# Optimization experiments

Hardware: AMD Instinct MI355X
Metric: run time of the kernel (lower is better)

## Reference

```python
import jax
import jax.numpy as jnp
import numpy as np

B, S, D, H, HID, E, TOPK = 1, 2048, 1024, 16, 4096, 8, 2
HEAD_DIM = D // H


def _layer_norm(x, g, b, eps=1e-5):
    mu = jnp.mean(x, axis=-1, keepdims=True)
    var = jnp.var(x, axis=-1, keepdims=True)
    return (x - mu) * jax.lax.rsqrt(var + eps) * g + b


def setup_inputs() -> dict:
    key = jax.random.key(0)
    ks = jax.random.split(key, 12)
    s = 0.02
    return {
        "x": jax.random.normal(ks[0], (B, S, D), jnp.float32),
        "ln1_g": jnp.ones((D,), jnp.float32),
        "ln1_b": jnp.zeros((D,), jnp.float32),
        "wq": jax.random.normal(ks[1], (D, D), jnp.float32) * s,
        "wk": jax.random.normal(ks[2], (D, D), jnp.float32) * s,
        "wv": jax.random.normal(ks[3], (D, D), jnp.float32) * s,
        "wo": jax.random.normal(ks[4], (D, D), jnp.float32) * s,
        "ln2_g": jnp.ones((D,), jnp.float32),
        "ln2_b": jnp.zeros((D,), jnp.float32),
        "w_gate": jax.random.normal(ks[5], (D, E), jnp.float32) * s,
        "w_eg": jax.random.normal(ks[6], (E, D, HID), jnp.float32) * s,
        "w_eu": jax.random.normal(ks[7], (E, D, HID), jnp.float32) * s,
        "w_ed": jax.random.normal(ks[8], (E, HID, D), jnp.float32) * s,
    }


def _attention(h, wq, wk, wv, wo):
    b, s, d = h.shape
    q = (h @ wq).reshape(b, s, H, HEAD_DIM).transpose(0, 2, 1, 3)
    k = (h @ wk).reshape(b, s, H, HEAD_DIM).transpose(0, 2, 1, 3)
    v = (h @ wv).reshape(b, s, H, HEAD_DIM).transpose(0, 2, 1, 3)
    scores = jnp.einsum("bhqd,bhkd->bhqk", q, k) / jnp.sqrt(jnp.asarray(HEAD_DIM, h.dtype))
    causal = jnp.tril(jnp.ones((s, s), bool))  # [s,s]
    scores = jnp.where(causal, scores, jnp.asarray(-1e30, h.dtype))
    attn = jax.nn.softmax(scores, axis=-1)
    out = jnp.einsum("bhqk,bhkd->bhqd", attn, v).transpose(0, 2, 1, 3).reshape(b, s, d)
    return out @ wo


def _moe(h, w_gate, w_eg, w_eu, w_ed):
    b, s, d = h.shape
    flat = h.reshape(-1, d)  # [T,D]
    logits = flat @ w_gate  # [T,E]
    scores = jax.nn.sigmoid(logits)
    top_val, top_idx = jax.lax.top_k(scores, TOPK)
    top_val = top_val / (jnp.sum(top_val, axis=-1, keepdims=True) + 1e-9)
    # per-token per-expert combine weight (0 for unrouted experts)
    combine = jnp.sum(jax.nn.one_hot(top_idx, E, dtype=flat.dtype) * top_val[..., None], axis=1)  # [T,E]
    g = jax.nn.silu(jnp.einsum("td,edh->eth", flat, w_eg))
    u = jnp.einsum("td,edh->eth", flat, w_eu)
    eo = jnp.einsum("eth,ehd->etd", g * u, w_ed)  # [E,T,D]
    out = jnp.einsum("etd,te->td", eo, combine)
    return out.reshape(b, s, d)


def reference(x, ln1_g, ln1_b, wq, wk, wv, wo, ln2_g, ln2_b, w_gate, w_eg, w_eu, w_ed):
    x = x + _attention(_layer_norm(x, ln1_g, ln1_b), wq, wk, wv, wo)
    x = x + _moe(_layer_norm(x, ln2_g, ln2_b), w_gate, w_eg, w_eu, w_ed)
    return x
```

## Files before the change

kernel.cpp:

```cpp
#include <hip/hip_runtime.h>
#include <stdint.h>

#define DI __device__ __forceinline__

typedef short bf16x8_t __attribute__((ext_vector_type(8)));
typedef float f32x4_t __attribute__((ext_vector_type(4)));

DI unsigned short f2bf(float f) {
  union { float f; uint32_t u; } v; v.f = f;
  uint32_t u = v.u;
  u += 0x7fffu + ((u >> 16) & 1u);
  return (unsigned short)(u >> 16);
}

DI f32x4_t mfma16(bf16x8_t a, bf16x8_t b, f32x4_t c) {
  return __builtin_amdgcn_mfma_f32_16x16x32_bf16(a, b, c, 0, 0, 0);
}

DI void gload16(const void* g, void* l) {
  __builtin_amdgcn_global_load_lds(
      (const __attribute__((address_space(1))) uint32_t*)g,
      (__attribute__((address_space(3))) uint32_t*)l, 16, 0, 0);
}

__global__ __launch_bounds__(256) void transpose_cvt(const float* __restrict__ in,
                                                     unsigned short* __restrict__ out,
                                                     int R, int C) {
  __shared__ float tile[64][65];
  const int tid = threadIdx.x;
  const int tx = tid & 15, ty = tid >> 4;
  const size_t zoff = (size_t)blockIdx.z * R * C;
  const int r0 = blockIdx.y * 64, c0 = blockIdx.x * 64;
#pragma unroll
  for (int i = 0; i < 4; ++i) {
    const int r = ty + i * 16;
    const float4 v = *(const float4*)(in + zoff + (size_t)(r0 + r) * C + c0 + tx * 4);
    tile[r][tx * 4 + 0] = v.x; tile[r][tx * 4 + 1] = v.y;
    tile[r][tx * 4 + 2] = v.z; tile[r][tx * 4 + 3] = v.w;
  }
  __syncthreads();
#pragma unroll
  for (int i = 0; i < 4; ++i) {
    const int r = ty + i * 16;
    ushort4 o;
    o.x = f2bf(tile[tx * 4 + 0][r]); o.y = f2bf(tile[tx * 4 + 1][r]);
    o.z = f2bf(tile[tx * 4 + 2][r]); o.w = f2bf(tile[tx * 4 + 3][r]);
    *(ushort4*)(out + zoff + (size_t)(c0 + r) * R + r0 + tx * 4) = o;
  }
}

__global__ __launch_bounds__(256) void ln_kernel(const float* __restrict__ x, const float* __restrict__ g,
                                                 const float* __restrict__ b, unsigned short* __restrict__ out) {
  const int row = blockIdx.x, tid = threadIdx.x;
  const int wid = tid >> 6, lane = tid & 63;
  const float4 v = *(const float4*)(x + (size_t)row * 1024 + tid * 4);
  float s = v.x + v.y + v.z + v.w;
  float s2 = v.x * v.x + v.y * v.y + v.z * v.z + v.w * v.w;
#pragma unroll
  for (int o = 1; o < 64; o <<= 1) { s += __shfl_xor(s, o); s2 += __shfl_xor(s2, o); }
  __shared__ float red[8];
  if (lane == 0) { red[wid] = s; red[4 + wid] = s2; }
  __syncthreads();
  const float ts = red[0] + red[1] + red[2] + red[3];
  const float ts2 = red[4] + red[5] + red[6] + red[7];
  const float mu = ts * 0.0009765625f;
  const float var = ts2 * 0.0009765625f - mu * mu;
  const float rs = rsqrtf(var + 1e-5f);
  const float4 gg = *(const float4*)(g + tid * 4);
  const float4 bb = *(const float4*)(b + tid * 4);
  ushort4 o4;
  o4.x = f2bf((v.x - mu) * rs * gg.x + bb.x);
  o4.y = f2bf((v.y - mu) * rs * gg.y + bb.y);
  o4.z = f2bf((v.z - mu) * rs * gg.z + bb.z);
  o4.w = f2bf((v.w - mu) * rs * gg.w + bb.w);
  *(ushort4*)(out + (size_t)row * 1024 + tid * 4) = o4;
}

template<int BN>
DI void gemm_loop(const unsigned short* aR0, const unsigned short* aR1,
                  const unsigned short* bR0, const unsigned short* bR1,
                  const int K, unsigned short* lds, const int tid,
                  f32x4_t (&acc)[4][BN / 32]) {
  constexpr int NF = BN / 32;
  unsigned short* ldsA = lds;
  unsigned short* ldsB = lds + 4096;
  const int wid = tid >> 6, lane = tid & 63, ln = lane & 15, hi = lane >> 4;
  const int wr = wid >> 1, wc = wid & 1;
  char* dstA0 = (char*)ldsA + wid * 1024;
  char* dstA1 = (char*)ldsA + 4096 + wid * 1024;
  char* dstB0 = (char*)ldsB + wid * 1024;
  char* dstB1 = (char*)ldsB + 4096 + wid * 1024;
  for (int k0 = 0; k0 < K; k0 += 32) {
    gload16(aR0 + k0, dstA0);
    gload16(aR1 + k0, dstA1);
    gload16(bR0 + k0, dstB0);
    if constexpr (BN == 128) gload16(bR1 + k0, dstB1);
    __syncthreads();
    bf16x8_t af[4];
#pragma unroll
    for (int mf = 0; mf < 4; ++mf)
      af[mf] = *(const bf16x8_t*)&ldsA[(wr * 64 + mf * 16 + ln) * 32 + hi * 8];
#pragma unroll
    for (int nf = 0; nf < NF; ++nf) {
      bf16x8_t bfr = *(const bf16x8_t*)&ldsB[(wc * (BN / 2) + nf * 16 + ln) * 32 + hi * 8];
#pragma unroll
      for (int mf = 0; mf < 4; ++mf)
        acc[mf][nf] = mfma16(af[mf], bfr, acc[mf][nf]);
    }
    __syncthreads();
  }
}

__global__ __launch_bounds__(256) void qkv_kernel(const unsigned short* __restrict__ h1,
                                                  const unsigned short* __restrict__ wqT,
                                                  const unsigned short* __restrict__ wkT,
                                                  const unsigned short* __restrict__ wvT,
                                                  unsigned short* __restrict__ qb,
                                                  unsigned short* __restrict__ kbf,
                                                  unsigned short* __restrict__ vt) {
  __shared__ unsigned short lds[128 * 32 + 128 * 32];
  const int tid = threadIdx.x;
  const int z = blockIdx.z;
  const unsigned short* BT = (z == 0) ? wqT : (z == 1) ? wkT : wvT;
  const int m0 = blockIdx.y * 128, n0 = blockIdx.x * 128;
  f32x4_t acc[4][4] = {};
  const unsigned short* aR0 = h1 + (size_t)(m0 + (tid >> 2)) * 1024 + (tid & 3) * 8;
  const unsigned short* aR1 = aR0 + 64 * 1024;
  const unsigned short* bR0 = BT + (size_t)(n0 + (tid >> 2)) * 1024 + (tid & 3) * 8;
  const unsigned short* bR1 = bR0 + 64 * 1024;
  gemm_loop<128>(aR0, aR1, bR0, bR1, 1024, lds, tid, acc);
  const int lane = tid & 63, ln = lane & 15, hi = lane >> 4, wid = tid >> 6;
  const int wr = wid >> 1, wc = wid & 1;
  if (z < 2) {
    unsigned short* o = z ? kbf : qb;
#pragma unroll
    for (int mf = 0; mf < 4; ++mf)
#pragma unroll
      for (int nf = 0; nf < 4; ++nf)
#pragma unroll
        for (int r = 0; r < 4; ++r) {
          const int m = m0 + wr * 64 + mf * 16 + hi * 4 + r;
          const int n = n0 + wc * 64 + nf * 16 + ln;
          o[(size_t)m * 1024 + n] = f2bf(acc[mf][nf][r]);
        }
  } else {
#pragma unroll
    for (int mf = 0; mf < 4; ++mf)
#pragma unroll
      for (int nf = 0; nf < 4; ++nf) {
        const int n = n0 + wc * 64 + nf * 16 + ln;
        const int mb = m0 + wr * 64 + mf * 16 + hi * 4;
        ushort4 o;
        o.x = f2bf(acc[mf][nf][0]); o.y = f2bf(acc[mf][nf][1]);
        o.z = f2bf(acc[mf][nf][2]); o.w = f2bf(acc[mf][nf][3]);
        *(ushort4*)(vt + (size_t)n * 2048 + mb) = o;
      }
  }
}

__global__ __launch_bounds__(256) void wo_kernel(const unsigned short* __restrict__ ao,
                                                 const unsigned short* __restrict__ woT,
                                                 const float* __restrict__ x,
                                                 float* __restrict__ out) {
  __shared__ unsigned short lds[128 * 32 + 64 * 32];
  const int tid = threadIdx.x;
  const int m0 = blockIdx.y * 128, n0 = blockIdx.x * 64;
  f32x4_t acc[4][2] = {};
  const unsigned short* aR0 = ao + (size_t)(m0 + (tid >> 2)) * 1024 + (tid & 3) * 8;
  const unsigned short* aR1 = aR0 + 64 * 1024;
  const unsigned short* bR0 = woT + (size_t)(n0 + (tid >> 2)) * 1024 + (tid & 3) * 8;
  gemm_loop<64>(aR0, aR1, bR0, nullptr, 1024, lds, tid, acc);
  const int lane = tid & 63, ln = lane & 15, hi = lane >> 4, wid = tid >> 6;
  const int wr = wid >> 1, wc = wid & 1;
#pragma unroll
  for (int mf = 0; mf < 4; ++mf)
#pragma unroll
    for (int nf = 0; nf < 2; ++nf)
#pragma unroll
      for (int r = 0; r < 4; ++r) {
        const int m = m0 + wr * 64 + mf * 16 + hi * 4 + r;
        const int n = n0 + wc * 32 + nf * 16 + ln;
        out[(size_t)m * 1024 + n] = acc[mf][nf][r] + x[(size_t)m * 1024 + n];
      }
}

__global__ __launch_bounds__(256) void attn_kernel(const unsigned short* __restrict__ qb,
                                                   const unsigned short* __restrict__ kbuf,
                                                   const unsigned short* __restrict__ vt,
                                                   unsigned short* __restrict__ ao) {
  __shared__ unsigned short kTl[4096];
  __shared__ unsigned short vTl[4096];
  __shared__ unsigned short pl[4][1024];
  const int tid = threadIdx.x;
  const int wid = tid >> 6, lane = tid & 63;
  const int ln = lane & 15, hi = lane >> 4;
  const int h = blockIdx.y;
  const int q0 = blockIdx.x * 64;
  const int q0w = q0 + wid * 16;

  const unsigned short* qrow = qb + (size_t)(q0w + ln) * 1024 + h * 64 + hi * 8;
  const bf16x8_t aq0 = *(const bf16x8_t*)(qrow);
  const bf16x8_t aq1 = *(const bf16x8_t*)(qrow + 32);

  const int str_r = tid >> 3, str_c = tid & 7;
  const int swc = (str_c ^ (str_r & 7)) * 8;
  const unsigned short* ksrc0 = kbuf + (size_t)str_r * 1024 + h * 64 + swc;
  const unsigned short* ksrc1 = kbuf + (size_t)(str_r + 32) * 1024 + h * 64 + swc;
  const unsigned short* vsrc0 = vt + (size_t)(h * 64 + str_r) * 2048 + swc;
  const unsigned short* vsrc1 = vt + (size_t)(h * 64 + str_r + 32) * 2048 + swc;
  char* kd0 = (char*)kTl + wid * 1024;
  char* kd1 = (char*)kTl + 4096 + wid * 1024;
  char* vd0 = (char*)vTl + wid * 1024;
  char* vd1 = (char*)vTl + 4096 + wid * 1024;

  float m_r[4], l_r[4];
  f32x4_t o_acc[4] = {};
#pragma unroll
  for (int r = 0; r < 4; ++r) { m_r[r] = -1e30f; l_r[r] = 0.f; }

  const int nkv = blockIdx.x + 1;
  for (int it = 0; it < nkv; ++it) {
    const int kv0 = it * 64;
    gload16(ksrc0 + (size_t)kv0 * 1024, kd0);
    gload16(ksrc1 + (size_t)kv0 * 1024, kd1);
    gload16(vsrc0 + kv0, vd0);
    gload16(vsrc1 + kv0, vd1);
    __syncthreads();

    float sc[4][4];
#pragma unroll
    for (int cf = 0; cf < 4; ++cf) {
      const int row = cf * 16 + ln;
      const int swz = row & 7;
      const bf16x8_t b0 = *(const bf16x8_t*)((char*)kTl + row * 128 + ((hi ^ swz) * 16));
      const bf16x8_t b1 = *(const bf16x8_t*)((char*)kTl + row * 128 + (((4 + hi) ^ swz) * 16));
      f32x4_t zacc = {};
      zacc = mfma16(aq0, b0, zacc);
      zacc = mfma16(aq1, b1, zacc);
#pragma unroll
      for (int r = 0; r < 4; ++r) sc[cf][r] = zacc[r] * 0.125f;
    }
    if (kv0 + 63 > q0w) {
#pragma unroll
      for (int cf = 0; cf < 4; ++cf)
#pragma unroll
        for (int r = 0; r < 4; ++r) {
          const int qg = q0w + hi * 4 + r;
          const int kg = kv0 + cf * 16 + ln;
          if (kg > qg) sc[cf][r] = -1e30f;
        }
    }
#pragma unroll
    for (int r = 0; r < 4; ++r) {
      float tm = fmaxf(fmaxf(sc[0][r], sc[1][r]), fmaxf(sc[2][r], sc[3][r]));
      tm = fmaxf(tm, __shfl_xor(tm, 1));
      tm = fmaxf(tm, __shfl_xor(tm, 2));
      tm = fmaxf(tm, __shfl_xor(tm, 4));
      tm = fmaxf(tm, __shfl_xor(tm, 8));
      const float mn = fmaxf(m_r[r], tm);
      const float alpha = __expf(m_r[r] - mn);
      float rsum = 0.f;
#pragma unroll
      for (int cf = 0; cf < 4; ++cf) {
        const float p = __expf(sc[cf][r] - mn);
        sc[cf][r] = p; rsum += p;
      }
      rsum += __shfl_xor(rsum, 1); rsum += __shfl_xor(rsum, 2);
      rsum += __shfl_xor(rsum, 4); rsum += __shfl_xor(rsum, 8);
      l_r[r] = l_r[r] * alpha + rsum;
      m_r[r] = mn;
#pragma unroll
      for (int df = 0; df < 4; ++df) o_acc[df][r] *= alpha;
    }
    unsigned short* pw = &pl[wid][0];
#pragma unroll
    for (int cf = 0; cf < 4; ++cf)
#pragma unroll
      for (int r = 0; r < 4; ++r) {
        const int qq = hi * 4 + r;
        const int kv = cf * 16 + ln;
        const int bo = (qq * 128 + kv * 2) ^ ((qq & 7) << 4);
        *(unsigned short*)((char*)pw + bo) = f2bf(sc[cf][r]);
      }
    __syncthreads();
    const bf16x8_t pa0 = *(const bf16x8_t*)((char*)pw + ((ln * 128 + hi * 16) ^ ((ln & 7) << 4)));
    const bf16x8_t pa1 = *(const bf16x8_t*)((char*)pw + ((ln * 128 + 64 + hi * 16) ^ ((ln & 7) << 4)));
#pragma unroll
    for (int df = 0; df < 4; ++df) {
      const int d = df * 16 + ln;
      const int swz = d & 7;
      const bf16x8_t bv0 = *(const bf16x8_t*)((char*)vTl + d * 128 + ((hi ^ swz) * 16));
      const bf16x8_t bv1 = *(const bf16x8_t*)((char*)vTl + d * 128 + (((4 + hi) ^ swz) * 16));
      o_acc[df] = mfma16(pa0, bv0, o_acc[df]);
      o_acc[df] = mfma16(pa1, bv1, o_acc[df]);
    }
    __syncthreads();
  }
#pragma unroll
  for (int df = 0; df < 4; ++df) {
    const int n = h * 64 + df * 16 + ln;
#pragma unroll
    for (int r = 0; r < 4; ++r) {
      const int m = q0w + hi * 4 + r;
      ao[(size_t)m * 1024 + n] = f2bf(o_acc[df][r] / l_r[r]);
    }
  }
}

__global__ __launch_bounds__(256) void gate_kernel(const float* __restrict__ x2, const float* __restrict__ g,
                                                   const float* __restrict__ b, const float* __restrict__ wg,
                                                   int2* __restrict__ te, float2* __restrict__ tw,
                                                   int* __restrict__ cnt) {
  const int tid = threadIdx.x, wid = tid >> 6, lane = tid & 63;
  const int t = blockIdx.x * 4 + wid;
  const float* row = x2 + (size_t)t * 1024;
  float vv[16];
#pragma unroll
  for (int i = 0; i < 4; ++i) *(float4*)&vv[i * 4] = *(const float4*)(row + lane * 16 + i * 4);
  float s = 0.f, s2 = 0.f;
#pragma unroll
  for (int j = 0; j < 16; ++j) { s += vv[j]; s2 += vv[j] * vv[j]; }
#pragma unroll
  for (int o = 1; o < 64; o <<= 1) { s += __shfl_xor(s, o); s2 += __shfl_xor(s2, o); }
  const float mu = s * 0.0009765625f;
  const float var = s2 * 0.0009765625f - mu * mu;
  const float rs = rsqrtf(var + 1e-5f);
  float acc[8] = {0.f, 0.f, 0.f, 0.f, 0.f, 0.f, 0.f, 0.f};
#pragma unroll
  for (int j = 0; j < 16; ++j) {
    const int d = lane * 16 + j;
    const float xv = (vv[j] - mu) * rs * g[d] + b[d];
    const float4 w0 = *(const float4*)(wg + d * 8);
    const float4 w1 = *(const float4*)(wg + d * 8 + 4);
    acc[0] += xv * w0.x; acc[1] += xv * w0.y; acc[2] += xv * w0.z; acc[3] += xv * w0.w;
    acc[4] += xv * w1.x; acc[5] += xv * w1.y; acc[6] += xv * w1.z; acc[7] += xv * w1.w;
  }
#pragma unroll
  for (int o = 1; o < 64; o <<= 1) {
#pragma unroll
    for (int e = 0; e < 8; ++e) acc[e] += __shfl_xor(acc[e], o);
  }
  if (lane == 0) {
    float sg[8];
#pragma unroll
    for (int e = 0; e < 8; ++e) sg[e] = 1.f / (1.f + __expf(-acc[e]));
    int e0 = 0;
#pragma unroll
    for (int e = 1; e < 8; ++e) if (sg[e] > sg[e0]) e0 = e;
    int e1 = (e0 == 0) ? 1 : 0;
#pragma unroll
    for (int e = 0; e < 8; ++e) if (e != e0 && sg[e] > sg[e1]) e1 = e;
    const float v0 = sg[e0], v1 = sg[e1];
    const float inv = 1.f / (v0 + v1 + 1e-9f);
    te[t] = make_int2(e0, e1);
    tw[t] = make_float2(v0 * inv, v1 * inv);
    atomicAdd(&cnt[e0], 1);
    atomicAdd(&cnt[e1], 1);
  }
}

__global__ void zero_counters(int* p) { if (threadIdx.x < 8) p[threadIdx.x] = 0; }

__global__ void g2_kernel(const int* __restrict__ cnt, int* __restrict__ slot_off,
                          int* __restrict__ tile_expert, int* __restrict__ tile_rowbase,
                          int* __restrict__ cursor, int* __restrict__ assign_token,
                          float* __restrict__ assign_w) {
  const int tid = threadIdx.x;
  for (int i = tid; i < 5120; i += 64) { assign_token[i] = -1; assign_w[i] = 0.f; }
  if (tid == 0) {
    int base = 0, tiles = 0;
    for (int e = 0; e < 8; ++e) {
      const int c = cnt[e];
      slot_off[e] = base;
      cursor[e] = 0;
      const int nt = (c + 127) >> 7;
      for (int i = 0; i < nt; ++i) {
        tile_expert[tiles] = e;
        tile_rowbase[tiles] = base + i * 128;
        ++tiles;
      }
      base += nt * 128;
    }
    for (; tiles < 40; ++tiles) tile_expert[tiles] = -1;
  }
}

__global__ __launch_bounds__(256) void g3_kernel(const int2* __restrict__ te, const float2* __restrict__ tw,
                                                 const int* __restrict__ slot_off, int* __restrict__ cursor,
                                                 int* __restrict__ assign_token, float* __restrict__ assign_w) {
  const int t = blockIdx.x * 256 + threadIdx.x;
  const int2 e = te[t];
  const float2 w = tw[t];
  const int s0 = slot_off[e.x] + atomicAdd(&cursor[e.x], 1);
  assign_token[s0] = t; assign_w[s0] = w.x;
  const int s1 = slot_off[e.y] + atomicAdd(&cursor[e.y], 1);
  assign_token[s1] = t; assign_w[s1] = w.y;
}

__global__ __launch_bounds__(256) void upgate_kernel(const unsigned short* __restrict__ h2,
                                                     const float* __restrict__ w_eg, const float* __restrict__ w_eu,
                                                     const int* __restrict__ tile_expert,
                                                     const int* __restrict__ tile_rowbase,
                                                     const int* __restrict__ assign_token,
                                                     unsigned short* __restrict__ act) {
  const int by = blockIdx.y;
  const int e = tile_expert[by];
  if (e < 0) return;
  const int n0 = blockIdx.x * 64;
  const int rowbase = tile_rowbase[by];
  const int tid = threadIdx.x;
  __shared__ unsigned short lds[128 * 32 + 2 * 64 * 32];
  unsigned short* ldsA = lds;
  unsigned short* ldsB = lds + 4096;
  const int wid = tid >> 6, lane = tid & 63, ln = lane & 15, hi = lane >> 4;
  const int wr = wid >> 1, wc = wid & 1;
  const int r0s = rowbase + (tid >> 2);
  int t0 = assign_token[r0s];       t0 = t0 < 0 ? 0 : t0;
  int t1 = assign_token[r0s + 64];  t1 = t1 < 0 ? 0 : t1;
  const unsigned short* aR0 = h2 + (size_t)t0 * 1024 + (tid & 3) * 8;
  const unsigned short* aR1 = h2 + (size_t)t1 * 1024 + (tid & 3) * 8;
  char* dstA0 = (char*)ldsA + wid * 1024;
  char* dstA1 = (char*)ldsA + 4096 + wid * 1024;
  const int mat = tid >> 7;
  const int blk = tid & 127;
  const int kb = (blk >> 4) * 4;
  const int nb = (blk & 15) * 4;
  const float* bsrc = (mat ? w_eu : w_eg) + (size_t)e * 1024 * 4096 + (size_t)kb * 4096 + n0 + nb;
  unsigned short* bdst[4];
#pragma unroll
  for (int i = 0; i < 4; ++i) {
    const int n = nb + i;
    int bo = mat * 4096 + n * 64 + kb * 2;
    bo ^= ((n >> 2) & 3) << 4;
    bdst[i] = (unsigned short*)((char*)ldsB + bo);
  }
  f32x4_t accg[4][2] = {};
  f32x4_t accu[4][2] = {};
  for (int k0 = 0; k0 < 1024; k0 += 32) {
    gload16(aR0 + k0, dstA0);
    gload16(aR1 + k0, dstA1);
    const float* bs = bsrc + (size_t)k0 * 4096;
    const float4 q0 = *(const float4*)(bs);
    const float4 q1 = *(const float4*)(bs + 4096);
    const float4 q2 = *(const float4*)(bs + 8192);
    const float4 q3 = *(const float4*)(bs + 12288);
    ushort4 w0, w1, w2, w3;
    w0.x = f2bf(q0.x); w0.y = f2bf(q1.x); w0.z = f2bf(q2.x); w0.w = f2bf(q3.x);
    w1.x = f2bf(q0.y); w1.y = f2bf(q1.y); w1.z = f2bf(q2.y); w1.w = f2bf(q3.y);
    w2.x = f2bf(q0.z); w2.y = f2bf(q1.z); w2.z = f2bf(q2.z); w2.w = f2bf(q3.z);
    w3.x = f2bf(q0.w); w3.y = f2bf(q1.w); w3.z = f2bf(q2.w); w3.w = f2bf(q3.w);
    *(ushort4*)bdst[0] = w0; *(ushort4*)bdst[1] = w1;
    *(ushort4*)bdst[2] = w2; *(ushort4*)bdst[3] = w3;
    __syncthreads();
    bf16x8_t af[4];
#pragma unroll
    for (int mf = 0; mf < 4; ++mf)
      af[mf] = *(const bf16x8_t*)&ldsA[(wr * 64 + mf * 16 + ln) * 32 + hi * 8];
#pragma unroll
    for (int nf = 0; nf < 2; ++nf) {
      const int nrow = wc * 32 + nf * 16 + ln;
      int bo = nrow * 64 + hi * 16;
      bo ^= ((nrow >> 2) & 3) << 4;
      const bf16x8_t bg = *(const bf16x8_t*)((char*)ldsB + bo);
      const bf16x8_t bu = *(const bf16x8_t*)((char*)ldsB + 4096 + bo);
#pragma unroll
      for (int mf = 0; mf < 4; ++mf) {
        accg[mf][nf] = mfma16(af[mf], bg, accg[mf][nf]);
        accu[mf][nf] = mfma16(af[mf], bu, accu[mf][nf]);
      }
    }
    __syncthreads();
  }
#pragma unroll
  for (int mf = 0; mf < 4; ++mf)
#pragma unroll
    for (int nf = 0; nf < 2; ++nf)
#pragma unroll
      for (int r = 0; r < 4; ++r) {
        const int m = wr * 64 + mf * 16 + hi * 4 + r;
        const int n = n0 + wc * 32 + nf * 16 + ln;
        const float gv = accg[mf][nf][r], uv = accu[mf][nf][r];
        const float val = gv / (1.f + __expf(-gv)) * uv;
        act[(size_t)(rowbase + m) * 4096 + n] = f2bf(val);
      }
}

__global__ __launch_bounds__(256) void down_kernel(const unsigned short* __restrict__ act,
                                                   const float* __restrict__ w_ed,
                                                   const int* __restrict__ tile_expert,
                                                   const int* __restrict__ tile_rowbase,
                                                   const int* __restrict__ assign_token,
                                                   const float* __restrict__ assign_w,
                                                   float* __restrict__ out) {
  const int by = blockIdx.y;
  const int e = tile_expert[by];
  if (e < 0) return;
  const int n0 = blockIdx.x * 64;
  const int rowbase = tile_rowbase[by];
  const int tid = threadIdx.x;
  __shared__ unsigned short lds[128 * 32 + 64 * 32];
  unsigned short* ldsA = lds;
  unsigned short* ldsB = lds + 4096;
  const int wid = tid >> 6, lane = tid & 63, ln = lane & 15, hi = lane >> 4;
  const int wr = wid >> 1, wc = wid & 1;
  const unsigned short* aR0 = act + (size_t)(rowbase + (tid >> 2)) * 4096 + (tid & 3) * 8;
  const unsigned short* aR1 = aR0 + (size_t)64 * 4096;
  char* dstA0 = (char*)ldsA + wid * 1024;
  char* dstA1 = (char*)ldsA + 4096 + wid * 1024;
  const int blk = tid & 127;
  const int kb = (blk >> 4) * 4;
  const int nb = (blk & 15) * 4;
  const float* bsrc = w_ed + (size_t)e * 4096 * 1024 + (size_t)kb * 1024 + n0 + nb;
  unsigned short* bdst[4];
#pragma unroll
  for (int i = 0; i < 4; ++i) {
    const int n = nb + i;
    int bo = n * 64 + kb * 2;
    bo ^= ((n >> 2) & 3) << 4;
    bdst[i] = (unsigned short*)((char*)ldsB + bo);
  }
  f32x4_t acc[4][2] = {};
  for (int k0 = 0; k0 < 4096; k0 += 32) {
    gload16(aR0 + k0, dstA0);
    gload16(aR1 + k0, dstA1);
    if (tid < 128) {
      const float* bs = bsrc + (size_t)k0 * 1024;
      const float4 q0 = *(const float4*)(bs);
      const float4 q1 = *(const float4*)(bs + 1024);
      const float4 q2 = *(const float4*)(bs + 2048);
      const float4 q3 = *(const float4*)(bs + 3072);
      ushort4 w0, w1, w2, w3;
      w0.x = f2bf(q0.x); w0.y = f2bf(q1.x); w0.z = f2bf(q2.x); w0.w = f2bf(q3.x);
      w1.x = f2bf(q0.y); w1.y = f2bf(q1.y); w1.z = f2bf(q2.y); w1.w = f2bf(q3.y);
      w2.x = f2bf(q0.z); w2.y = f2bf(q1.z); w2.z = f2bf(q2.z); w2.w = f2bf(q3.z);
      w3.x = f2bf(q0.w); w3.y = f2bf(q1.w); w3.z = f2bf(q2.w); w3.w = f2bf(q3.w);
      *(ushort4*)bdst[0] = w0; *(ushort4*)bdst[1] = w1;
      *(ushort4*)bdst[2] = w2; *(ushort4*)bdst[3] = w3;
    }
    __syncthreads();
    bf16x8_t af[4];
#pragma unroll
    for (int mf = 0; mf < 4; ++mf)
      af[mf] = *(const bf16x8_t*)&ldsA[(wr * 64 + mf * 16 + ln) * 32 + hi * 8];
#pragma unroll
    for (int nf = 0; nf < 2; ++nf) {
      const int nrow = wc * 32 + nf * 16 + ln;
      int bo = nrow * 64 + hi * 16;
      bo ^= ((nrow >> 2) & 3) << 4;
      const bf16x8_t bb = *(const bf16x8_t*)((char*)ldsB + bo);
#pragma unroll
      for (int mf = 0; mf < 4; ++mf)
        acc[mf][nf] = mfma16(af[mf], bb, acc[mf][nf]);
    }
    __syncthreads();
  }
#pragma unroll
  for (int mf = 0; mf < 4; ++mf)
#pragma unroll
    for (int r = 0; r < 4; ++r) {
      const int m = wr * 64 + mf * 16 + hi * 4 + r;
      const int slot = rowbase + m;
      const int tk = assign_token[slot];
      if (tk >= 0) {
        const float w = assign_w[slot];
#pragma unroll
        for (int nf = 0; nf < 2; ++nf) {
          const int n = n0 + wc * 32 + nf * 16 + ln;
          atomicAdd(out + (size_t)tk * 1024 + n, acc[mf][nf][r] * w);
        }
      }
    }
}

extern "C" void kernel_launch(void* const* d_in, const int* in_sizes, int n_in,
                              void* d_out, int out_size, void* d_ws, size_t ws_size,
                              hipStream_t stream) {
  (void)in_sizes; (void)n_in; (void)out_size;
  const float* x    = (const float*)d_in[0];
  const float* ln1g = (const float*)d_in[1];
  const float* ln1b = (const float*)d_in[2];
  const float* wq   = (const float*)d_in[3];
  const float* wk   = (const float*)d_in[4];
  const float* wv   = (const float*)d_in[5];
  const float* wo   = (const float*)d_in[6];
  const float* ln2g = (const float*)d_in[7];
  const float* ln2b = (const float*)d_in[8];
  const float* wg   = (const float*)d_in[9];
  const float* weg  = (const float*)d_in[10];
  const float* weu  = (const float*)d_in[11];
  const float* wed  = (const float*)d_in[12];
  float* out = (float*)d_out;
  char* ws = (char*)d_ws;

  const size_t MB = (size_t)1 << 20;
  if (ws_size < 74 * MB) return;
  unsigned short* wqT = (unsigned short*)(ws + 0 * MB);
  unsigned short* wkT = (unsigned short*)(ws + 2 * MB);
  unsigned short* wvT = (unsigned short*)(ws + 4 * MB);
  unsigned short* woT = (unsigned short*)(ws + 6 * MB);
  unsigned short* h1  = (unsigned short*)(ws + 8 * MB);
  unsigned short* qb  = (unsigned short*)(ws + 12 * MB);
  unsigned short* kbf = (unsigned short*)(ws + 16 * MB);
  unsigned short* vt  = (unsigned short*)(ws + 20 * MB);
  unsigned short* ao  = (unsigned short*)(ws + 24 * MB);
  unsigned short* h2  = (unsigned short*)(ws + 28 * MB);
  unsigned short* act = (unsigned short*)(ws + 32 * MB);
  int2*   te = (int2*)(ws + 72 * MB);
  float2* tw = (float2*)(ws + 72 * MB + 16384);
  int*  meta = (int*)(ws + 72 * MB + 32768);
  int* cnt = meta;
  int* cursor = meta + 8;
  int* slot_off = meta + 16;
  int* tile_expert = meta + 24;
  int* tile_rowbase = meta + 64;
  int*   assign_token = (int*)(ws + 72 * MB + 36864);
  float* assign_w     = (float*)(ws + 72 * MB + 36864 + 20480);

  zero_counters<<<1, 64, 0, stream>>>(cnt);
  transpose_cvt<<<dim3(16, 16, 1), 256, 0, stream>>>(wq, wqT, 1024, 1024);
  transpose_cvt<<<dim3(16, 16, 1), 256, 0, stream>>>(wk, wkT, 1024, 1024);
  transpose_cvt<<<dim3(16, 16, 1), 256, 0, stream>>>(wv, wvT, 1024, 1024);
  transpose_cvt<<<dim3(16, 16, 1), 256, 0, stream>>>(wo, woT, 1024, 1024);
  ln_kernel<<<2048, 256, 0, stream>>>(x, ln1g, ln1b, h1);
  qkv_kernel<<<dim3(8, 16, 3), 256, 0, stream>>>(h1, wqT, wkT, wvT, qb, kbf, vt);
  attn_kernel<<<dim3(32, 16), 256, 0, stream>>>(qb, kbf, vt, ao);
  wo_kernel<<<dim3(16, 16), 256, 0, stream>>>(ao, woT, x, out);
  ln_kernel<<<2048, 256, 0, stream>>>(out, ln2g, ln2b, h2);
  gate_kernel<<<512, 256, 0, stream>>>(out, ln2g, ln2b, wg, te, tw, cnt);
  g2_kernel<<<1, 64, 0, stream>>>(cnt, slot_off, tile_expert, tile_rowbase, cursor, assign_token, assign_w);
  g3_kernel<<<8, 256, 0, stream>>>(te, tw, slot_off, cursor, assign_token, assign_w);
  upgate_kernel<<<dim3(64, 40), 256, 0, stream>>>(h2, weg, weu, tile_expert, tile_rowbase, assign_token, act);
  down_kernel<<<dim3(16, 40), 256, 0, stream>>>(act, wed, tile_expert, tile_rowbase, assign_token, assign_w, out);
}
```

Baseline: 527.1 us.

## Swizzle LDS tiles to cut bank conflicts and spread down-proj weight conversion

```diff
diff --git a/kernel.cpp b/kernel.cpp
--- a/kernel.cpp
+++ b/kernel.cpp
@@ -1,4 +1,5 @@
 #include <hip/hip_runtime.h>
+#include <hip/hip_bf16.h>
 #include <stdint.h>
 
 #define DI __device__ __forceinline__
@@ -7,10 +8,14 @@
 typedef float f32x4_t __attribute__((ext_vector_type(4)));
 
 DI unsigned short f2bf(float f) {
-  union { float f; uint32_t u; } v; v.f = f;
-  uint32_t u = v.u;
-  u += 0x7fffu + ((u >> 16) & 1u);
-  return (unsigned short)(u >> 16);
+  __hip_bfloat16 h = __float2bfloat16(f);
+  unsigned short u;
+  __builtin_memcpy(&u, &h, 2);
+  return u;
+}
+
+DI uint32_t pk2(float a, float b) {
+  return (uint32_t)f2bf(a) | ((uint32_t)f2bf(b) << 16);
 }
 
 DI f32x4_t mfma16(bf16x8_t a, bf16x8_t b, f32x4_t c) {
@@ -22,6 +27,11 @@
       (const __attribute__((address_space(1))) uint32_t*)g,
       (__attribute__((address_space(3))) uint32_t*)l, 16, 0, 0);
 }
+
+DI bf16x8_t frag(const unsigned short* base, int row, int hi) {
+  return *(const bf16x8_t*)&base[row * 32 + ((hi ^ ((row >> 1) & 3)) * 8)];
+}
+DI int chunk_swz(int tid) { return ((tid & 3) ^ ((tid >> 3) & 3)) * 8; }
 
 __global__ __launch_bounds__(256) void transpose_cvt(const float* __restrict__ in,
                                                      unsigned short* __restrict__ out,
@@ -99,10 +109,10 @@
     bf16x8_t af[4];
 #pragma unroll
     for (int mf = 0; mf < 4; ++mf)
-      af[mf] = *(const bf16x8_t*)&ldsA[(wr * 64 + mf * 16 + ln) * 32 + hi * 8];
+      af[mf] = frag(ldsA, wr * 64 + mf * 16 + ln, hi);
 #pragma unroll
     for (int nf = 0; nf < NF; ++nf) {
-      bf16x8_t bfr = *(const bf16x8_t*)&ldsB[(wc * (BN / 2) + nf * 16 + ln) * 32 + hi * 8];
+      bf16x8_t bfr = frag(ldsB, wc * (BN / 2) + nf * 16 + ln, hi);
 #pragma unroll
       for (int mf = 0; mf < 4; ++mf)
         acc[mf][nf] = mfma16(af[mf], bfr, acc[mf][nf]);
@@ -124,9 +134,10 @@
   const unsigned short* BT = (z == 0) ? wqT : (z == 1) ? wkT : wvT;
   const int m0 = blockIdx.y * 128, n0 = blockIdx.x * 128;
   f32x4_t acc[4][4] = {};
-  const unsigned short* aR0 = h1 + (size_t)(m0 + (tid >> 2)) * 1024 + (tid & 3) * 8;
+  const int cs = chunk_swz(tid);
+  const unsigned short* aR0 = h1 + (size_t)(m0 + (tid >> 2)) * 1024 + cs;
   const unsigned short* aR1 = aR0 + 64 * 1024;
-  const unsigned short* bR0 = BT + (size_t)(n0 + (tid >> 2)) * 1024 + (tid & 3) * 8;
+  const unsigned short* bR0 = BT + (size_t)(n0 + (tid >> 2)) * 1024 + cs;
   const unsigned short* bR1 = bR0 + 64 * 1024;
   gemm_loop<128>(aR0, aR1, bR0, bR1, 1024, lds, tid, acc);
   const int lane = tid & 63, ln = lane & 15, hi = lane >> 4, wid = tid >> 6;
@@ -166,9 +177,10 @@
   const int tid = threadIdx.x;
   const int m0 = blockIdx.y * 128, n0 = blockIdx.x * 64;
   f32x4_t acc[4][2] = {};
-  const unsigned short* aR0 = ao + (size_t)(m0 + (tid >> 2)) * 1024 + (tid & 3) * 8;
+  const int cs = chunk_swz(tid);
+  const unsigned short* aR0 = ao + (size_t)(m0 + (tid >> 2)) * 1024 + cs;
   const unsigned short* aR1 = aR0 + 64 * 1024;
-  const unsigned short* bR0 = woT + (size_t)(n0 + (tid >> 2)) * 1024 + (tid & 3) * 8;
+  const unsigned short* bR0 = woT + (size_t)(n0 + (tid >> 2)) * 1024 + cs;
   gemm_loop<64>(aR0, aR1, bR0, nullptr, 1024, lds, tid, acc);
   const int lane = tid & 63, ln = lane & 15, hi = lane >> 4, wid = tid >> 6;
   const int wr = wid >> 1, wc = wid & 1;
@@ -417,8 +429,9 @@
   const int r0s = rowbase + (tid >> 2);
   int t0 = assign_token[r0s];       t0 = t0 < 0 ? 0 : t0;
   int t1 = assign_token[r0s + 64];  t1 = t1 < 0 ? 0 : t1;
-  const unsigned short* aR0 = h2 + (size_t)t0 * 1024 + (tid & 3) * 8;
-  const unsigned short* aR1 = h2 + (size_t)t1 * 1024 + (tid & 3) * 8;
+  const int cs = chunk_swz(tid);
+  const unsigned short* aR0 = h2 + (size_t)t0 * 1024 + cs;
+  const unsigned short* aR1 = h2 + (size_t)t1 * 1024 + cs;
   char* dstA0 = (char*)ldsA + wid * 1024;
   char* dstA1 = (char*)ldsA + 4096 + wid * 1024;
   const int mat = tid >> 7;
@@ -426,13 +439,13 @@
   const int kb = (blk >> 4) * 4;
   const int nb = (blk & 15) * 4;
   const float* bsrc = (mat ? w_eu : w_eg) + (size_t)e * 1024 * 4096 + (size_t)kb * 4096 + n0 + nb;
-  unsigned short* bdst[4];
+  char* bdst[4];
 #pragma unroll
   for (int i = 0; i < 4; ++i) {
     const int n = nb + i;
     int bo = mat * 4096 + n * 64 + kb * 2;
-    bo ^= ((n >> 2) & 3) << 4;
-    bdst[i] = (unsigned short*)((char*)ldsB + bo);
+    bo ^= ((n >> 2) & 7) << 4;
+    bdst[i] = (char*)ldsB + bo;
   }
   f32x4_t accg[4][2] = {};
   f32x4_t accu[4][2] = {};
@@ -444,23 +457,25 @@
     const float4 q1 = *(const float4*)(bs + 4096);
     const float4 q2 = *(const float4*)(bs + 8192);
     const float4 q3 = *(const float4*)(bs + 12288);
-    ushort4 w0, w1, w2, w3;
-    w0.x = f2bf(q0.x); w0.y = f2bf(q1.x); w0.z = f2bf(q2.x); w0.w = f2bf(q3.x);
-    w1.x = f2bf(q0.y); w1.y = f2bf(q1.y); w1.z = f2bf(q2.y); w1.w = f2bf(q3.y);
-    w2.x = f2bf(q0.z); w2.y = f2bf(q1.z); w2.z = f2bf(q2.z); w2.w = f2bf(q3.z);
-    w3.x = f2bf(q0.w); w3.y = f2bf(q1.w); w3.z = f2bf(q2.w); w3.w = f2bf(q3.w);
-    *(ushort4*)bdst[0] = w0; *(ushort4*)bdst[1] = w1;
-    *(ushort4*)bdst[2] = w2; *(ushort4*)bdst[3] = w3;
+    const float* q0p = (const float*)&q0; const float* q1p = (const float*)&q1;
+    const float* q2p = (const float*)&q2; const float* q3p = (const float*)&q3;
+#pragma unroll
+    for (int i = 0; i < 4; ++i) {
+      uint2 w;
+      w.x = pk2(q0p[i], q1p[i]);
+      w.y = pk2(q2p[i], q3p[i]);
+      *(uint2*)bdst[i] = w;
+    }
     __syncthreads();
     bf16x8_t af[4];
 #pragma unroll
     for (int mf = 0; mf < 4; ++mf)
-      af[mf] = *(const bf16x8_t*)&ldsA[(wr * 64 + mf * 16 + ln) * 32 + hi * 8];
+      af[mf] = frag(ldsA, wr * 64 + mf * 16 + ln, hi);
 #pragma unroll
     for (int nf = 0; nf < 2; ++nf) {
       const int nrow = wc * 32 + nf * 16 + ln;
       int bo = nrow * 64 + hi * 16;
-      bo ^= ((nrow >> 2) & 3) << 4;
+      bo ^= ((nrow >> 2) & 7) << 4;
       const bf16x8_t bg = *(const bf16x8_t*)((char*)ldsB + bo);
       const bf16x8_t bu = *(const bf16x8_t*)((char*)ldsB + 4096 + bo);
 #pragma unroll
@@ -503,50 +518,50 @@
   unsigned short* ldsB = lds + 4096;
   const int wid = tid >> 6, lane = tid & 63, ln = lane & 15, hi = lane >> 4;
   const int wr = wid >> 1, wc = wid & 1;
-  const unsigned short* aR0 = act + (size_t)(rowbase + (tid >> 2)) * 4096 + (tid & 3) * 8;
+  const int cs = chunk_swz(tid);
+  const unsigned short* aR0 = act + (size_t)(rowbase + (tid >> 2)) * 4096 + cs;
   const unsigned short* aR1 = aR0 + (size_t)64 * 4096;
   char* dstA0 = (char*)ldsA + wid * 1024;
   char* dstA1 = (char*)ldsA + 4096 + wid * 1024;
-  const int blk = tid & 127;
-  const int kb = (blk >> 4) * 4;
-  const int nb = (blk & 15) * 4;
+  const int nb = (tid & 31) * 2;
+  const int kb = (tid >> 5) * 4;
   const float* bsrc = w_ed + (size_t)e * 4096 * 1024 + (size_t)kb * 1024 + n0 + nb;
-  unsigned short* bdst[4];
-#pragma unroll
-  for (int i = 0; i < 4; ++i) {
-    const int n = nb + i;
+  char* bdst[2];
+#pragma unroll
+  for (int j = 0; j < 2; ++j) {
+    const int n = nb + j;
     int bo = n * 64 + kb * 2;
-    bo ^= ((n >> 2) & 3) << 4;
-    bdst[i] = (unsigned short*)((char*)ldsB + bo);
+    bo ^= ((n >> 2) & 7) << 4;
+    bdst[j] = (char*)ldsB + bo;
   }
   f32x4_t acc[4][2] = {};
   for (int k0 = 0; k0 < 4096; k0 += 32) {
     gload16(aR0 + k0, dstA0);
     gload16(aR1 + k0, dstA1);
-    if (tid < 128) {
-      const float* bs = bsrc + (size_t)k0 * 1024;
-      const float4 q0 = *(const float4*)(bs);
-      const float4 q1 = *(const float4*)(bs + 1024);
-      const float4 q2 = *(const float4*)(bs + 2048);
-      const float4 q3 = *(const float4*)(bs + 3072);
-      ushort4 w0, w1, w2, w3;
-      w0.x = f2bf(q0.x); w0.y = f2bf(q1.x); w0.z = f2bf(q2.x); w0.w = f2bf(q3.x);
-      w1.x = f2bf(q0.y); w1.y = f2bf(q1.y); w1.z = f2bf(q2.y); w1.w = f2bf(q3.y);
-      w2.x = f2bf(q0.z); w2.y = f2bf(q1.z); w2.z = f2bf(q2.z); w2.w = f2bf(q3.z);
-      w3.x = f2bf(q0.w); w3.y = f2bf(q1.w); w3.z = f2bf(q2.w); w3.w = f2bf(q3.w);
-      *(ushort4*)bdst[0] = w0; *(ushort4*)bdst[1] = w1;
-      *(ushort4*)bdst[2] = w2; *(ushort4*)bdst[3] = w3;
+    const float* bs = bsrc + (size_t)k0 * 1024;
+    const float2 q0 = *(const float2*)(bs);
+    const float2 q1 = *(const float2*)(bs + 1024);
+    const float2 q2 = *(const float2*)(bs + 2048);
+    const float2 q3 = *(const float2*)(bs + 3072);
+    const float* q0p = (const float*)&q0; const float* q1p = (const float*)&q1;
+    const float* q2p = (const float*)&q2; const float* q3p = (const float*)&q3;
+#pragma unroll
+    for (int j = 0; j < 2; ++j) {
+      uint2 w;
+      w.x = pk2(q0p[j], q1p[j]);
+      w.y = pk2(q2p[j], q3p[j]);
+      *(uint2*)bdst[j] = w;
     }
     __syncthreads();
     bf16x8_t af[4];
 #pragma unroll
     for (int mf = 0; mf < 4; ++mf)
-      af[mf] = *(const bf16x8_t*)&ldsA[(wr * 64 + mf * 16 + ln) * 32 + hi * 8];
+      af[mf] = frag(ldsA, wr * 64 + mf * 16 + ln, hi);
 #pragma unroll
     for (int nf = 0; nf < 2; ++nf) {
       const int nrow = wc * 32 + nf * 16 + ln;
       int bo = nrow * 64 + hi * 16;
-      bo ^= ((nrow >> 2) & 3) << 4;
+      bo ^= ((nrow >> 2) & 7) << 4;
       const bf16x8_t bb = *(const bf16x8_t*)((char*)ldsB + bo);
 #pragma unroll
       for (int mf = 0; mf < 4; ++mf)
```

After: 508.2 us. -3.6%, faster.
